# Performance work log

Hardware: AMD Instinct MI355X
Metric: run time of the kernel (lower is better)

The kernel has to match this reference:

```python
import jax, jax.numpy as jnp
import numpy as np

DT = 0.01          # discretization timestep (init kwarg dt)
DAMP_MIN = 5e-4    # minimum damping (init kwarg damp_min)
BATCH, SEQ, D_IN, N_STATE = 16, 2048, 1024, 128


def setup_inputs() -> dict:
    key = jax.random.key(0)
    k1, k2, k3, k4, k5 = jax.random.split(key, 5)
    u = jax.random.normal(k1, (BATCH, SEQ, D_IN), jnp.float32)
    # A_real init: randn*0.1 - damp_min, then clamped to <= -damp_min (stability)
    A_real = jnp.minimum(jax.random.normal(k2, (N_STATE,), jnp.float32) * 0.1 - DAMP_MIN, -DAMP_MIN)
    A_imag = jax.random.normal(k3, (N_STATE,), jnp.float32)
    B = jax.random.normal(k4, (N_STATE, D_IN), jnp.float32) * 0.02
    C = jax.random.normal(k5, (D_IN, N_STATE), jnp.float32) * 0.02
    return {"u": u, "A_real": A_real, "A_imag": A_imag, "B": B, "C": C}


def reference(u, A_real, A_imag, B, C):
    """Real-input path of StableResonantSSM.

    Bilinear discretization of diagonal complex A:
      a_disc = (1 + dt/2 * a) / (1 - dt/2 * a)          (elementwise, A diagonal)
      B_disc = sqrt(dt) * B / (1 - dt/2 * a)            (row-wise scaling)
    Recurrence: h_t = a_disc * h_{t-1} + B_disc @ u_t;  y_t = Re(C @ h_t).
    """
    dt = jnp.float32(DT)
    a = (A_real + 1j * A_imag).astype(jnp.complex64)          # (N,)
    denom = 1.0 - (dt / 2) * a                                 # (N,) complex
    a_disc = (1.0 + (dt / 2) * a) / denom                      # (N,)
    B_disc = (jnp.sqrt(dt) * B.astype(jnp.complex64)) / denom[:, None]  # (N, D)

    # Precompute all input injections as one GEMM: (T, B, N) complex
    Bu = jnp.einsum('btd,nd->tbn', u, B_disc)

    def step(h, bu_t):
        h = a_disc * h + bu_t
        return h, h

    h0 = jnp.zeros((u.shape[0], a.shape[0]), jnp.complex64)
    _, hs = jax.lax.scan(step, h0, Bu)                         # hs: (T, B, N)

    # C is real, so Re(C @ h) == C @ Re(h)
    y = jnp.einsum('tbn,dn->btd', hs.real, C)                  # (B, T, D)
    return y
```

## Files before the change

kernel.cpp:

```cpp
#include <hip/hip_runtime.h>
#include <hip/hip_bf16.h>
#include <cstdint>

#define DT_F    0.01f
#define NB      16
#define T_SEQ   2048
#define DD      1024
#define NS      128
#define CHUNK   64
#define NCH     32

using f32x4  = __attribute__((ext_vector_type(4))) float;
using bf16x8 = __attribute__((ext_vector_type(8))) short;
using fl4    = __attribute__((ext_vector_type(4))) float;

#define AS1(p) ((const __attribute__((address_space(1))) void*)(p))
#define AS3(p) ((__attribute__((address_space(3))) void*)(p))

__device__ __forceinline__ unsigned short f2bf(float f) {
  union { float f; unsigned u; } v; v.f = f;
  unsigned r = v.u + 0x7fffu + ((v.u >> 16) & 1u);
  return (unsigned short)(r >> 16);
}
__device__ __forceinline__ float bf2f(unsigned short s) {
  union { unsigned u; float f; } v; v.u = ((unsigned)s) << 16;
  return v.f;
}
__device__ __forceinline__ unsigned short f2bf_hw(float f) {
  __hip_bfloat16 h = __float2bfloat16(f);
  return __builtin_bit_cast(unsigned short, h);
}

__device__ __forceinline__ void adisc(float Arn, float Ain, float& ar, float& ai) {
  const float dr = 1.f - 0.5f * DT_F * Arn;
  const float di = -0.5f * DT_F * Ain;
  const float inv = 1.f / (dr * dr + di * di);
  const float nr = 1.f + 0.5f * DT_F * Arn;
  const float nim = 0.5f * DT_F * Ain;
  ar = (nr * dr + nim * di) * inv;
  ai = (nim * dr - nr * di) * inv;
}

__global__ void prep_all(const float* __restrict__ Ar, const float* __restrict__ Ai,
                         const float* __restrict__ B, const float* __restrict__ C,
                         unsigned short* __restrict__ W, unsigned short* __restrict__ Cb) {
  const int blk = blockIdx.x;
  const int tid = threadIdx.x;
  if (blk < 512) {
    const int i = blk * 256 + tid;
    Cb[i] = f2bf(C[i]);
    return;
  }
  const int n = blk - 512;
  const float ar = Ar[n], ai = Ai[n];
  const float dr = 1.f - 0.5f * DT_F * ar;
  const float di = -0.5f * DT_F * ai;
  const float inv = 1.f / (dr * dr + di * di);
  const float s  = sqrtf(DT_F);
  const float cr = s * dr * inv;
  const float ci = -s * di * inv;
  for (int d = tid; d < DD; d += 256) {
    const float b = B[(size_t)n * DD + d];
    W[(size_t)n * DD + d]        = f2bf(b * cr);
    W[(size_t)(NS + n) * DD + d] = f2bf(b * ci);
  }
}

__global__ __launch_bounds__(256, 2) void gemm1s(const float* __restrict__ U,
                                                 const float* __restrict__ Ar,
                                                 const float* __restrict__ Ai,
                                                 const unsigned short* __restrict__ W,
                                                 unsigned short* __restrict__ Hs,
                                                 float* __restrict__ F) {
  __shared__ __align__(16) char smem[40960];
  unsigned short* As = (unsigned short*)smem;
  unsigned short* Bs = (unsigned short*)(smem + 8192);
  char*           Bt = smem;

  const int tid  = threadIdx.x;
  const int lane = tid & 63;
  const int wave = tid >> 6;
  const int blk  = blockIdx.x;
  const size_t m0 = (size_t)blk * CHUNK;

  f32x4 acc[4][4];
  const f32x4 zero = {0.f, 0.f, 0.f, 0.f};
#pragma unroll
  for (int i = 0; i < 4; ++i)
#pragma unroll
    for (int j = 0; j < 4; ++j) acc[i][j] = zero;

  const int srow  = tid >> 2;
  const int scol  = (tid & 3) * 16;
  const int growl = lane >> 3;
  const int gcol  = (lane & 7) * 8;

  for (int k0 = 0; k0 < DD; k0 += 64) {
    __syncthreads();
#pragma unroll
    for (int g = 0; g < 8; ++g) {
      const int row = wave * 64 + g * 8;
      const unsigned short* gb = W + (size_t)(row + growl) * DD + k0 + gcol;
      __builtin_amdgcn_global_load_lds(AS1(gb), AS3(&Bs[row * 64]), 16, 0, 0);
    }
    {
      const float* ga = U + (m0 + srow) * DD + k0 + scol;
      fl4 v0 = *(const fl4*)ga;
      fl4 v1 = *(const fl4*)(ga + 4);
      fl4 v2 = *(const fl4*)(ga + 8);
      fl4 v3 = *(const fl4*)(ga + 12);
      bf16x8 p0, p1;
#pragma unroll
      for (int e = 0; e < 4; ++e) {
        p0[e] = (short)f2bf_hw(v0[e]); p0[4 + e] = (short)f2bf_hw(v1[e]);
        p1[e] = (short)f2bf_hw(v2[e]); p1[4 + e] = (short)f2bf_hw(v3[e]);
      }
      *(bf16x8*)&As[srow * 64 + scol]     = p0;
      *(bf16x8*)&As[srow * 64 + scol + 8] = p1;
    }
    __syncthreads();
#pragma unroll
    for (int ks = 0; ks < 2; ++ks) {
      bf16x8 af[4], bfr[4];
#pragma unroll
      for (int i = 0; i < 4; ++i)
        af[i] = *(const bf16x8*)&As[(i * 16 + (lane & 15)) * 64 + ks * 32 + (lane >> 4) * 8];
#pragma unroll
      for (int j = 0; j < 4; ++j)
        bfr[j] = *(const bf16x8*)&Bs[(wave * 64 + j * 16 + (lane & 15)) * 64 + ks * 32 + (lane >> 4) * 8];
#pragma unroll
      for (int i = 0; i < 4; ++i)
#pragma unroll
        for (int j = 0; j < 4; ++j)
          acc[i][j] = __builtin_amdgcn_mfma_f32_16x16x32_bf16(af[i], bfr[j], acc[i][j], 0, 0, 0);
    }
  }
  __syncthreads();

#pragma unroll
  for (int i = 0; i < 4; ++i) {
#pragma unroll
    for (int j = 0; j < 4; ++j) {
      const int cc = wave * 64 + j * 16 + (lane & 15);
#pragma unroll
      for (int q = 0; q < 4; ++q) {
        const int t = i * 16 + (lane >> 4) * 4 + q;
        *(unsigned short*)(Bt + t * 512 + ((cc * 2) ^ ((t & 7) << 4))) = f2bf_hw(acc[i][j][q]);
      }
    }
  }
  __syncthreads();

  if (tid < 128) {
    const int n = tid;
    float ar, ai; adisc(Ar[n], Ai[n], ar, ai);
    float hr = 0.f, hi = 0.f;
    unsigned short* o = Hs + (size_t)blk * (CHUNK * NS) + n;
#pragma unroll 8
    for (int t = 0; t < CHUNK; ++t) {
      const int reByte = t * 512 + ((n * 2) ^ ((t & 7) << 4));
      const float br = bf2f(*(const unsigned short*)(Bt + reByte));
      const float bi = bf2f(*(const unsigned short*)(Bt + reByte + 256));
      const float xr = fmaf(ar, hr, fmaf(-ai, hi, br));
      const float xi = fmaf(ar, hi, fmaf(ai, hr, bi));
      hr = xr; hi = xi;
      o[t * NS] = f2bf(hr);
    }
    F[(size_t)blk * 256 + n]       = hr;
    F[(size_t)blk * 256 + 128 + n] = hi;
  }
}

__global__ void carry_scan(const float* __restrict__ F,
                           const float* __restrict__ Ar, const float* __restrict__ Ai,
                           float* __restrict__ G) {
  const int b = blockIdx.x;
  const int n = threadIdx.x;
  float ar, ai; adisc(Ar[n], Ai[n], ar, ai);
  float alr = ar, ali = ai;
#pragma unroll
  for (int s = 0; s < 6; ++s) {
    const float tr = alr * alr - ali * ali;
    const float ti = 2.f * alr * ali;
    alr = tr; ali = ti;
  }
  float cr = 0.f, ci = 0.f;
  for (int c = 0; c < NCH; ++c) {
    const size_t idx = ((size_t)b * NCH + c) * 256 + n;
    G[idx]       = ar * cr - ai * ci;
    G[idx + 128] = ar * ci + ai * cr;
    const float fr = F[idx];
    const float fi = F[idx + 128];
    const float xr = fmaf(alr, cr, fmaf(-ali, ci, fr));
    const float xi = fmaf(alr, ci, fmaf(ali, cr, fi));
    cr = xr; ci = xi;
  }
}

__global__ __launch_bounds__(256, 2) void gemm2s(const unsigned short* __restrict__ Hs,
                                                 const float* __restrict__ G,
                                                 const float* __restrict__ Ar,
                                                 const float* __restrict__ Ai,
                                                 const unsigned short* __restrict__ Cb,
                                                 float* __restrict__ y) {
  __shared__ __align__(16) char Hl[64 * 256];
  const int tid  = threadIdx.x;
  const int lane = tid & 63;
  const int wave = tid >> 6;
  const int blk  = blockIdx.x;
  const int c    = blk & 31;
  const size_t m0 = (size_t)blk * CHUNK;

  const char* tile = (const char*)Hs + (size_t)blk * (CHUNK * NS * 2);
#pragma unroll
  for (int g = 0; g < 4; ++g) {
    const int r0 = wave * 16 + g * 4;
    const int r  = r0 + (lane >> 4);
    const int srcOff = r * 256 + ((((lane & 15)) * 16) ^ ((r & 7) << 4));
    __builtin_amdgcn_global_load_lds(AS1(tile + srcOff), AS3(Hl + r0 * 256), 16, 0, 0);
  }
  __syncthreads();

  if (c != 0 && tid < 128) {
    const int n = tid;
    float ar, ai; adisc(Ar[n], Ai[n], ar, ai);
    float gr = G[(size_t)blk * 256 + n];
    float gi = G[(size_t)blk * 256 + 128 + n];
#pragma unroll 8
    for (int t = 0; t < CHUNK; ++t) {
      unsigned short* pp = (unsigned short*)(Hl + t * 256 + ((n * 2) ^ ((t & 7) << 4)));
      *pp = f2bf(bf2f(*pp) + gr);
      const float xr = ar * gr - ai * gi;
      const float xi = ar * gi + ai * gr;
      gr = xr; gi = xi;
    }
  }
  __syncthreads();

  const f32x4 zero = {0.f, 0.f, 0.f, 0.f};
#pragma unroll
  for (int cg = 0; cg < 4; ++cg) {
    const int d0 = wave * 256 + cg * 64;
    f32x4 oacc[4][4];
#pragma unroll
    for (int i = 0; i < 4; ++i)
#pragma unroll
      for (int j = 0; j < 4; ++j) oacc[i][j] = zero;

#pragma unroll
    for (int ks = 0; ks < 4; ++ks) {
      bf16x8 af[4], bfr[4];
#pragma unroll
      for (int i = 0; i < 4; ++i) {
        const int r = i * 16 + (lane & 15);
        af[i] = *(const bf16x8*)(Hl + r * 256 + ((ks * 64 + (lane >> 4) * 16) ^ ((r & 7) << 4)));
      }
#pragma unroll
      for (int j = 0; j < 4; ++j)
        bfr[j] = *(const bf16x8*)(Cb + (size_t)(d0 + j * 16 + (lane & 15)) * NS + ks * 32 + (lane >> 4) * 8);
#pragma unroll
      for (int i = 0; i < 4; ++i)
#pragma unroll
        for (int j = 0; j < 4; ++j)
          oacc[i][j] = __builtin_amdgcn_mfma_f32_16x16x32_bf16(af[i], bfr[j], oacc[i][j], 0, 0, 0);
    }
#pragma unroll
    for (int i = 0; i < 4; ++i) {
      const size_t r0 = m0 + i * 16 + (lane >> 4) * 4;
#pragma unroll
      for (int j = 0; j < 4; ++j) {
        const int d = d0 + j * 16 + (lane & 15);
#pragma unroll
        for (int q = 0; q < 4; ++q)
          y[(r0 + q) * DD + d] = oacc[i][j][q];
      }
    }
  }
}

extern "C" void kernel_launch(void* const* d_in, const int* in_sizes, int n_in,
                              void* d_out, int out_size, void* d_ws, size_t ws_size,
                              hipStream_t stream) {
  const float* u  = (const float*)d_in[0];
  const float* Ar = (const float*)d_in[1];
  const float* Ai = (const float*)d_in[2];
  const float* B  = (const float*)d_in[3];
  const float* C  = (const float*)d_in[4];
  float* y = (float*)d_out;
  char* ws = (char*)d_ws;

  unsigned short* W  = (unsigned short*)(ws);
  unsigned short* Cb = (unsigned short*)(ws + (512 << 10));
  float*          F  = (float*)(ws + (768 << 10));
  float*          G  = (float*)(ws + (1280 << 10));
  unsigned short* Hs = (unsigned short*)(ws + (1792 << 10));

  prep_all<<<dim3(640), dim3(256), 0, stream>>>(Ar, Ai, B, C, W, Cb);
  gemm1s<<<dim3(NB * NCH), dim3(256), 0, stream>>>(u, Ar, Ai, W, Hs, F);
  carry_scan<<<dim3(NB), dim3(128), 0, stream>>>(F, Ar, Ai, G);
  gemm2s<<<dim3(NB * NCH), dim3(256), 0, stream>>>(Hs, G, Ar, Ai, Cb, y);
}
```

Before: 84.08 us.

## Factor complex B scaling out of GEMM1 to halve its N dimension

Because B_disc is a real B scaled row-wise by a complex per-state factor, GEMM1 now multiplies u by the real bf16 B (128 outputs instead of 256). The complex factor (cr, ci) is applied inside the scan loop. This halves the MFMA work, the B tile loads and the LDS footprint in gemm1s, and simplifies the prep kernel. The cost is two extra multiplies per scan step and a change in where bf16 rounding happens: the GEMM result is rounded before it is scaled.

```diff
diff --git a/kernel.cpp b/kernel.cpp
--- a/kernel.cpp
+++ b/kernel.cpp
@@ -31,7 +31,9 @@
   return __builtin_bit_cast(unsigned short, h);
 }
 
-__device__ __forceinline__ void adisc(float Arn, float Ain, float& ar, float& ai) {
+__device__ __forceinline__ void adisc_full(float Arn, float Ain,
+                                           float& ar, float& ai,
+                                           float& cr, float& ci) {
   const float dr = 1.f - 0.5f * DT_F * Arn;
   const float di = -0.5f * DT_F * Ain;
   const float inv = 1.f / (dr * dr + di * di);
@@ -39,40 +41,34 @@
   const float nim = 0.5f * DT_F * Ain;
   ar = (nr * dr + nim * di) * inv;
   ai = (nim * dr - nr * di) * inv;
-}
-
-__global__ void prep_all(const float* __restrict__ Ar, const float* __restrict__ Ai,
-                         const float* __restrict__ B, const float* __restrict__ C,
-                         unsigned short* __restrict__ W, unsigned short* __restrict__ Cb) {
+  const float s = sqrtf(DT_F);
+  cr = s * dr * inv;
+  ci = -s * di * inv;
+}
+__device__ __forceinline__ void adisc(float Arn, float Ain, float& ar, float& ai) {
+  float cr, ci; adisc_full(Arn, Ain, ar, ai, cr, ci);
+}
+
+__global__ void prep_all(const float* __restrict__ B, const float* __restrict__ C,
+                         unsigned short* __restrict__ Bb, unsigned short* __restrict__ Cb) {
   const int blk = blockIdx.x;
   const int tid = threadIdx.x;
   if (blk < 512) {
     const int i = blk * 256 + tid;
     Cb[i] = f2bf(C[i]);
-    return;
-  }
-  const int n = blk - 512;
-  const float ar = Ar[n], ai = Ai[n];
-  const float dr = 1.f - 0.5f * DT_F * ar;
-  const float di = -0.5f * DT_F * ai;
-  const float inv = 1.f / (dr * dr + di * di);
-  const float s  = sqrtf(DT_F);
-  const float cr = s * dr * inv;
-  const float ci = -s * di * inv;
-  for (int d = tid; d < DD; d += 256) {
-    const float b = B[(size_t)n * DD + d];
-    W[(size_t)n * DD + d]        = f2bf(b * cr);
-    W[(size_t)(NS + n) * DD + d] = f2bf(b * ci);
+  } else {
+    const int i = (blk - 512) * 256 + tid;
+    Bb[i] = f2bf(B[i]);
   }
 }
 
 __global__ __launch_bounds__(256, 2) void gemm1s(const float* __restrict__ U,
                                                  const float* __restrict__ Ar,
                                                  const float* __restrict__ Ai,
-                                                 const unsigned short* __restrict__ W,
+                                                 const unsigned short* __restrict__ Bb,
                                                  unsigned short* __restrict__ Hs,
                                                  float* __restrict__ F) {
-  __shared__ __align__(16) char smem[40960];
+  __shared__ __align__(16) char smem[24576];
   unsigned short* As = (unsigned short*)smem;
   unsigned short* Bs = (unsigned short*)(smem + 8192);
   char*           Bt = smem;
@@ -83,12 +79,12 @@
   const int blk  = blockIdx.x;
   const size_t m0 = (size_t)blk * CHUNK;
 
-  f32x4 acc[4][4];
+  f32x4 acc[4][2];
   const f32x4 zero = {0.f, 0.f, 0.f, 0.f};
 #pragma unroll
   for (int i = 0; i < 4; ++i)
 #pragma unroll
-    for (int j = 0; j < 4; ++j) acc[i][j] = zero;
+    for (int j = 0; j < 2; ++j) acc[i][j] = zero;
 
   const int srow  = tid >> 2;
   const int scol  = (tid & 3) * 16;
@@ -98,9 +94,9 @@
   for (int k0 = 0; k0 < DD; k0 += 64) {
     __syncthreads();
 #pragma unroll
-    for (int g = 0; g < 8; ++g) {
-      const int row = wave * 64 + g * 8;
-      const unsigned short* gb = W + (size_t)(row + growl) * DD + k0 + gcol;
+    for (int g = 0; g < 4; ++g) {
+      const int row = wave * 32 + g * 8;
+      const unsigned short* gb = Bb + (size_t)(row + growl) * DD + k0 + gcol;
       __builtin_amdgcn_global_load_lds(AS1(gb), AS3(&Bs[row * 64]), 16, 0, 0);
     }
     {
@@ -121,17 +117,17 @@
     __syncthreads();
 #pragma unroll
     for (int ks = 0; ks < 2; ++ks) {
-      bf16x8 af[4], bfr[4];
+      bf16x8 af[4], bfr[2];
 #pragma unroll
       for (int i = 0; i < 4; ++i)
         af[i] = *(const bf16x8*)&As[(i * 16 + (lane & 15)) * 64 + ks * 32 + (lane >> 4) * 8];
 #pragma unroll
-      for (int j = 0; j < 4; ++j)
-        bfr[j] = *(const bf16x8*)&Bs[(wave * 64 + j * 16 + (lane & 15)) * 64 + ks * 32 + (lane >> 4) * 8];
+      for (int j = 0; j < 2; ++j)
+        bfr[j] = *(const bf16x8*)&Bs[(wave * 32 + j * 16 + (lane & 15)) * 64 + ks * 32 + (lane >> 4) * 8];
 #pragma unroll
       for (int i = 0; i < 4; ++i)
 #pragma unroll
-        for (int j = 0; j < 4; ++j)
+        for (int j = 0; j < 2; ++j)
           acc[i][j] = __builtin_amdgcn_mfma_f32_16x16x32_bf16(af[i], bfr[j], acc[i][j], 0, 0, 0);
     }
   }
@@ -140,12 +136,12 @@
 #pragma unroll
   for (int i = 0; i < 4; ++i) {
 #pragma unroll
-    for (int j = 0; j < 4; ++j) {
-      const int cc = wave * 64 + j * 16 + (lane & 15);
+    for (int j = 0; j < 2; ++j) {
+      const int n = wave * 32 + j * 16 + (lane & 15);
 #pragma unroll
       for (int q = 0; q < 4; ++q) {
         const int t = i * 16 + (lane >> 4) * 4 + q;
-        *(unsigned short*)(Bt + t * 512 + ((cc * 2) ^ ((t & 7) << 4))) = f2bf_hw(acc[i][j][q]);
+        *(unsigned short*)(Bt + t * 256 + ((n * 2) ^ ((t & 7) << 4))) = f2bf_hw(acc[i][j][q]);
       }
     }
   }
@@ -153,14 +149,14 @@
 
   if (tid < 128) {
     const int n = tid;
-    float ar, ai; adisc(Ar[n], Ai[n], ar, ai);
+    float ar, ai, cr, ci; adisc_full(Ar[n], Ai[n], ar, ai, cr, ci);
     float hr = 0.f, hi = 0.f;
     unsigned short* o = Hs + (size_t)blk * (CHUNK * NS) + n;
 #pragma unroll 8
     for (int t = 0; t < CHUNK; ++t) {
-      const int reByte = t * 512 + ((n * 2) ^ ((t & 7) << 4));
-      const float br = bf2f(*(const unsigned short*)(Bt + reByte));
-      const float bi = bf2f(*(const unsigned short*)(Bt + reByte + 256));
+      const float s = bf2f(*(const unsigned short*)(Bt + t * 256 + ((n * 2) ^ ((t & 7) << 4))));
+      const float br = cr * s;
+      const float bi = ci * s;
       const float xr = fmaf(ar, hr, fmaf(-ai, hi, br));
       const float xi = fmaf(ar, hi, fmaf(ai, hr, bi));
       hr = xr; hi = xi;
@@ -289,14 +285,14 @@
   float* y = (float*)d_out;
   char* ws = (char*)d_ws;
 
-  unsigned short* W  = (unsigned short*)(ws);
-  unsigned short* Cb = (unsigned short*)(ws + (512 << 10));
-  float*          F  = (float*)(ws + (768 << 10));
-  float*          G  = (float*)(ws + (1280 << 10));
-  unsigned short* Hs = (unsigned short*)(ws + (1792 << 10));
-
-  prep_all<<<dim3(640), dim3(256), 0, stream>>>(Ar, Ai, B, C, W, Cb);
-  gemm1s<<<dim3(NB * NCH), dim3(256), 0, stream>>>(u, Ar, Ai, W, Hs, F);
+  unsigned short* Bb = (unsigned short*)(ws);
+  unsigned short* Cb = (unsigned short*)(ws + (256 << 10));
+  float*          F  = (float*)(ws + (512 << 10));
+  float*          G  = (float*)(ws + (1024 << 10));
+  unsigned short* Hs = (unsigned short*)(ws + (1536 << 10));
+
+  prep_all<<<dim3(1024), dim3(256), 0, stream>>>(B, C, Bb, Cb);
+  gemm1s<<<dim3(NB * NCH), dim3(256), 0, stream>>>(u, Ar, Ai, Bb, Hs, F);
   carry_scan<<<dim3(NB), dim3(128), 0, stream>>>(F, Ar, Ai, G);
   gemm2s<<<dim3(NB * NCH), dim3(256), 0, stream>>>(Hs, G, Ar, Ai, Cb, y);
 }
```

Result: faster. 75.82 us (-9.8%).
